# Optimization experiments

Hardware: AMD Instinct MI355X
Metric: run time of the kernel (lower is better)

## Reference

```python
import jax, jax.numpy as jnp
import numpy as np

N_HEADS = 16
D_HEAD = 64
N_ROTATE = 32
ROPE_BASE = 10000.0
MAX_LEN = 2048  # round_up_to_multiple_of_256(keep count); static for jit
BATCH, SEQ = 2, 4096


def setup_inputs() -> dict:
    key = jax.random.key(0)
    kq, kk, kv = jax.random.split(key, 3)
    q = jax.random.normal(kq, (BATCH, N_HEADS, MAX_LEN, D_HEAD), jnp.float32)
    k = jax.random.normal(kk, (BATCH, N_HEADS, SEQ, D_HEAD), jnp.float32)
    v = jax.random.normal(kv, (BATCH, N_HEADS, SEQ, D_HEAD), jnp.float32)
    # causal full mask [batch, seq, seq] and full position ids [batch, seq]
    mask_full = jnp.broadcast_to(jnp.tril(jnp.ones((SEQ, SEQ), bool)), (BATCH, SEQ, SEQ))
    pos_full = jnp.broadcast_to(jnp.arange(SEQ, dtype=jnp.int32), (BATCH, SEQ))
    # skip_mask: exactly MAX_LEN kept tokens per row (random positions)
    rng = np.random.default_rng(0)
    sm = np.zeros((BATCH, SEQ), dtype=bool)
    for i in range(BATCH):
        sm[i, rng.permutation(SEQ)[:MAX_LEN]] = True
    return {"q": q, "k": k, "v": v, "mask_full": mask_full,
            "pos_full": pos_full, "skip_mask": jnp.asarray(sm)}


def _rope_rotate(x, pos):
    # x: [b, h, L, n_rotate], pos: [b, L]
    half = N_ROTATE // 2
    inv_freq = 1.0 / (ROPE_BASE ** (jnp.arange(0, N_ROTATE, 2, dtype=jnp.float32) / N_ROTATE))
    freqs = pos.astype(jnp.float32)[..., None] * inv_freq          # [b, L, half]
    emb = jnp.concatenate([freqs, freqs], axis=-1)[:, None]        # [b, 1, L, n_rotate]
    cos, sin = jnp.cos(emb), jnp.sin(emb)
    x1, x2 = x[..., :half], x[..., half:]
    rot = jnp.concatenate([-x2, x1], axis=-1)                      # rotate_half
    return x * cos + rot * sin


def reference(q, k, v, mask_full, pos_full, skip_mask):
    b, S = skip_mask.shape
    lengths = skip_mask.sum(axis=1)
    # vectorized _trim_attention_mask: stable argsort compacts kept indices to the front
    order = jnp.argsort(jnp.where(skip_mask, 0, 1), axis=1, stable=True)
    idx = order[:, :MAX_LEN]                                       # [b, max_len]
    brow = jnp.arange(b)[:, None]
    mask_trim = mask_full[brow, idx]                               # [b, max_len, S]
    pos_trim = pos_full[brow, idx]                                 # [b, max_len]
    valid = jnp.arange(MAX_LEN)[None, :] < lengths[:, None]
    mask_trim = mask_trim & valid[..., None]
    pos_trim = jnp.where(valid, pos_trim, 0)

    # partial RoPE on first n_rotate channels
    rq = _rope_rotate(q[..., :N_ROTATE], pos_trim)
    rk = _rope_rotate(k[..., :N_ROTATE], pos_full)
    q = jnp.concatenate([rq, q[..., N_ROTATE:]], axis=-1)
    k = jnp.concatenate([rk, k[..., N_ROTATE:]], axis=-1)

    # masked SDPA (bool mask broadcast over heads)
    scale = 1.0 / jnp.sqrt(jnp.float32(D_HEAD))
    scores = jnp.einsum('bhqd,bhkd->bhqk', q, k) * scale
    scores = jnp.where(mask_trim[:, None], scores, jnp.finfo(scores.dtype).min)
    attn = jax.nn.softmax(scores, axis=-1)
    return jnp.einsum('bhqk,bhkd->bhqd', attn, v)
```

## Files before the change

kernel.cpp:

```cpp
#include <hip/hip_runtime.h>
#include <math.h>

#define BB 2
#define HH 16
#define QQ 2048
#define SS 4096
#define DD 64
#define NRH 16
#define NQT 32
#define PBPAD 68

typedef unsigned short u16;
typedef unsigned int   u32;
typedef short bhalf8 __attribute__((ext_vector_type(8)));
typedef float f32x4  __attribute__((ext_vector_type(4)));

typedef __attribute__((address_space(1))) const u32 gu32;
typedef __attribute__((address_space(3))) u32 lu32;

#if __has_builtin(__builtin_amdgcn_exp2f)
#define EXP2(x) __builtin_amdgcn_exp2f(x)
#else
#define EXP2(x) exp2f(x)
#endif

union Frag16 { uint4 u; bhalf8 v; u16 s[8]; uint2 d[2]; };

__device__ __forceinline__ u16 f2bf(float f) {
  union { float f; u32 u; } c; c.f = f;
  return (u16)((c.u + 0x7FFFu + ((c.u >> 16) & 1u)) >> 16);
}

__device__ __forceinline__ bhalf8 ldfrag(const u16* p) {
  Frag16 f; f.u = *reinterpret_cast<const uint4*>(p); return f.v;
}

__device__ __forceinline__ void rope32(float* x, int pos) {
  const float step = 0.8304820237218405f;
  const float fp = (float)pos;
#pragma unroll
  for (int i = 0; i < NRH; ++i) {
    float ang = fp * exp2f(-step * (float)i);
    float sv, cv;
    __sincosf(ang, &sv, &cv);
    float a = x[i], b = x[i + NRH];
    x[i]       = a * cv - b * sv;
    x[i + NRH] = b * cv + a * sv;
  }
}

__global__ void prep_idx_kernel(const unsigned char* __restrict__ sm,
                                int* __restrict__ idx) {
  __shared__ int wsum[4];
  __shared__ int modes;
  const int tid = threadIdx.x;
  const int b = (int)blockIdx.x;

  int c = 0;
  for (int i = 0; i < 32; ++i) c += (sm[tid * 32 + i] != 0) ? 1 : 0;
#pragma unroll
  for (int off = 32; off; off >>= 1) c += __shfl_down(c, off);
  if ((tid & 63) == 0) wsum[tid >> 6] = c;
  __syncthreads();
  if (tid == 0) modes = (wsum[0] + wsum[1] + wsum[2] + wsum[3] > 3000) ? 1 : 0;
  __syncthreads();
  const bool byteMode = (modes != 0);
  const u32* sm32 = (const u32*)sm;

  const int base = b * SS + tid * 16;
  u32 flags = 0;
  for (int i = 0; i < 16; ++i) {
    bool f = byteMode ? (sm[base + i] != 0) : (sm32[base + i] != 0);
    flags |= ((u32)(f ? 1 : 0)) << i;
  }
  int cnt = __popc(flags);
  int vv = cnt;
#pragma unroll
  for (int off = 1; off < 64; off <<= 1) {
    int t = __shfl_up(vv, off);
    if ((tid & 63) >= off) vv += t;
  }
  __syncthreads();
  if ((tid & 63) == 63) wsum[tid >> 6] = vv;
  __syncthreads();
  int add = 0;
  for (int w2 = 0; w2 < (tid >> 6); ++w2) add += wsum[w2];
  int p = vv - cnt + add;
  for (int i = 0; i < 16; ++i) {
    if (flags & (1u << i)) {
      if (p < QQ) idx[b * QQ + p] = tid * 16 + i;
      ++p;
    }
  }
}

__global__ __launch_bounds__(256) void prep_kv_kernel(const float* __restrict__ k,
                                                      const float* __restrict__ v,
                                                      u16* __restrict__ kbf,
                                                      u16* __restrict__ vt) {
  __shared__ u16 tile[64][72];
  if (blockIdx.x < 512) {
    int r = blockIdx.x * 256 + threadIdx.x;
    int pos = r & (SS - 1);
    float x[64];
    const float4* src = (const float4*)(k + (size_t)r * DD);
#pragma unroll
    for (int i = 0; i < 16; ++i) {
      float4 t = src[i];
      x[4 * i] = t.x; x[4 * i + 1] = t.y; x[4 * i + 2] = t.z; x[4 * i + 3] = t.w;
    }
    rope32(x, pos);
    u16 tmp[64];
#pragma unroll
    for (int i = 0; i < 64; ++i) tmp[i] = f2bf(x[i]);
    uint4* dst = (uint4*)(kbf + (size_t)r * DD);
#pragma unroll
    for (int i = 0; i < 8; ++i) dst[i] = ((uint4*)tmp)[i];
  } else {
    int blk = (int)blockIdx.x - 512;
    int bh = blk >> 6;
    int jt = blk & 63;
    int t = threadIdx.x;
    int jl = t >> 2;
    int dc = (t & 3) * 16;
    const float4* src = (const float4*)(v + ((size_t)(bh * SS + jt * 64 + jl)) * DD + dc);
#pragma unroll
    for (int i = 0; i < 4; ++i) {
      float4 f = src[i];
      tile[jl][dc + 4 * i]     = f2bf(f.x);
      tile[jl][dc + 4 * i + 1] = f2bf(f.y);
      tile[jl][dc + 4 * i + 2] = f2bf(f.z);
      tile[jl][dc + 4 * i + 3] = f2bf(f.w);
    }
    __syncthreads();
    int d = t >> 2;
    int js = (t & 3) * 16;
    u16 o[16];
#pragma unroll
    for (int i = 0; i < 16; ++i) o[i] = tile[js + i][d];
    uint4* dst = (uint4*)(vt + ((size_t)(bh * DD + d)) * SS + jt * 64 + js);
    dst[0] = ((uint4*)o)[0];
    dst[1] = ((uint4*)o)[1];
  }
}

__device__ __forceinline__ void stage_tiles(const char* kb_bh, const char* vt_bh,
                                            u16* Kb, u16* Vb, int t0,
                                            int w, int srow, int schk) {
#pragma unroll
  for (int p2 = 0; p2 < 2; ++p2) {
    const int rr = w * 16 + p2 * 8 + srow;
    {
      const char* g = kb_bh + (size_t)(t0 + rr) * 128 + ((schk ^ (rr & 7)) * 16);
      lu32* l = (lu32*)((char*)Kb + (w * 16 + p2 * 8) * 128);
      __builtin_amdgcn_global_load_lds((gu32*)g, l, 16, 0, 0);
    }
    {
      const char* g = vt_bh + (size_t)rr * (SS * 2) + t0 * 2 + ((schk ^ (rr & 7)) * 16);
      lu32* l = (lu32*)((char*)Vb + (w * 16 + p2 * 8) * 128);
      __builtin_amdgcn_global_load_lds((gu32*)g, l, 16, 0, 0);
    }
  }
}

__device__ __forceinline__ void attn_tile(
    const u16* __restrict__ Kb, const u16* __restrict__ Vb, u16* __restrict__ pb,
    int t0, int grp, int col,
    int bnd0, int bnd1, int bnd2, int bnd3,
    bhalf8 qa0, bhalf8 qa1,
    f32x4& acc0, f32x4& acc1, f32x4& acc2, f32x4& acc3,
    float& l0, float& l1, float& l2, float& l3) {
  const int swz = col & 7;
  f32x4 s0 = {0.f, 0.f, 0.f, 0.f}, s1 = s0, s2 = s0, s3 = s0;
  {
    const u16* kr0 = Kb + (0 * 16 + col) * 64;
    const u16* kr1 = Kb + (1 * 16 + col) * 64;
    const u16* kr2 = Kb + (2 * 16 + col) * 64;
    const u16* kr3 = Kb + (3 * 16 + col) * 64;
    s0 = __builtin_amdgcn_mfma_f32_16x16x32_bf16(qa0, ldfrag(kr0 + ((grp ^ swz) * 8)), s0, 0, 0, 0);
    s1 = __builtin_amdgcn_mfma_f32_16x16x32_bf16(qa0, ldfrag(kr1 + ((grp ^ swz) * 8)), s1, 0, 0, 0);
    s2 = __builtin_amdgcn_mfma_f32_16x16x32_bf16(qa0, ldfrag(kr2 + ((grp ^ swz) * 8)), s2, 0, 0, 0);
    s3 = __builtin_amdgcn_mfma_f32_16x16x32_bf16(qa0, ldfrag(kr3 + ((grp ^ swz) * 8)), s3, 0, 0, 0);
    s0 = __builtin_amdgcn_mfma_f32_16x16x32_bf16(qa1, ldfrag(kr0 + (((4 + grp) ^ swz) * 8)), s0, 0, 0, 0);
    s1 = __builtin_amdgcn_mfma_f32_16x16x32_bf16(qa1, ldfrag(kr1 + (((4 + grp) ^ swz) * 8)), s1, 0, 0, 0);
    s2 = __builtin_amdgcn_mfma_f32_16x16x32_bf16(qa1, ldfrag(kr2 + (((4 + grp) ^ swz) * 8)), s2, 0, 0, 0);
    s3 = __builtin_amdgcn_mfma_f32_16x16x32_bf16(qa1, ldfrag(kr3 + (((4 + grp) ^ swz) * 8)), s3, 0, 0, 0);
  }

  const int key0 = t0 + col, key1 = t0 + 16 + col, key2 = t0 + 32 + col, key3 = t0 + 48 + col;
#define SM_ROW(R, BND, LACC)                                                   \
  {                                                                            \
    float p0 = (key0 <= (BND)) ? EXP2(s0[R] - 16.f) : 0.f;                     \
    float p1 = (key1 <= (BND)) ? EXP2(s1[R] - 16.f) : 0.f;                     \
    float p2v = (key2 <= (BND)) ? EXP2(s2[R] - 16.f) : 0.f;                    \
    float p3 = (key3 <= (BND)) ? EXP2(s3[R] - 16.f) : 0.f;                     \
    (LACC) += (p0 + p1) + (p2v + p3);                                          \
    u16* prow = pb + (grp * 4 + (R)) * PBPAD;                                  \
    prow[col] = f2bf(p0); prow[16 + col] = f2bf(p1);                           \
    prow[32 + col] = f2bf(p2v); prow[48 + col] = f2bf(p3);                     \
  }
  SM_ROW(0, bnd0, l0)
  SM_ROW(1, bnd1, l1)
  SM_ROW(2, bnd2, l2)
  SM_ROW(3, bnd3, l3)
#undef SM_ROW

  bhalf8 pa0, pa1;
  {
    const u16* p = pb + col * PBPAD;
    Frag16 f0, f1;
    f0.d[0] = *(const uint2*)(p + grp * 8);
    f0.d[1] = *(const uint2*)(p + grp * 8 + 4);
    f1.d[0] = *(const uint2*)(p + 32 + grp * 8);
    f1.d[1] = *(const uint2*)(p + 32 + grp * 8 + 4);
    pa0 = f0.v; pa1 = f1.v;
  }

  {
    const u16* vr0 = Vb + (0 * 16 + col) * 64;
    const u16* vr1 = Vb + (1 * 16 + col) * 64;
    const u16* vr2 = Vb + (2 * 16 + col) * 64;
    const u16* vr3 = Vb + (3 * 16 + col) * 64;
    acc0 = __builtin_amdgcn_mfma_f32_16x16x32_bf16(pa0, ldfrag(vr0 + ((grp ^ swz) * 8)), acc0, 0, 0, 0);
    acc1 = __builtin_amdgcn_mfma_f32_16x16x32_bf16(pa0, ldfrag(vr1 + ((grp ^ swz) * 8)), acc1, 0, 0, 0);
    acc2 = __builtin_amdgcn_mfma_f32_16x16x32_bf16(pa0, ldfrag(vr2 + ((grp ^ swz) * 8)), acc2, 0, 0, 0);
    acc3 = __builtin_amdgcn_mfma_f32_16x16x32_bf16(pa0, ldfrag(vr3 + ((grp ^ swz) * 8)), acc3, 0, 0, 0);
    acc0 = __builtin_amdgcn_mfma_f32_16x16x32_bf16(pa1, ldfrag(vr0 + (((4 + grp) ^ swz) * 8)), acc0, 0, 0, 0);
    acc1 = __builtin_amdgcn_mfma_f32_16x16x32_bf16(pa1, ldfrag(vr1 + (((4 + grp) ^ swz) * 8)), acc1, 0, 0, 0);
    acc2 = __builtin_amdgcn_mfma_f32_16x16x32_bf16(pa1, ldfrag(vr2 + (((4 + grp) ^ swz) * 8)), acc2, 0, 0, 0);
    acc3 = __builtin_amdgcn_mfma_f32_16x16x32_bf16(pa1, ldfrag(vr3 + (((4 + grp) ^ swz) * 8)), acc3, 0, 0, 0);
  }
}

__global__ __launch_bounds__(256) void attn_mfma_kernel(
    const float* __restrict__ qsrc, const u16* __restrict__ kbf,
    const u16* __restrict__ vt, const int* __restrict__ idx,
    float* __restrict__ out) {
  __shared__ u16 KbufA[64 * 64];
  __shared__ u16 VbufA[64 * 64];
  __shared__ u16 KbufB[64 * 64];
  __shared__ u16 VbufB[64 * 64];
  __shared__ u16 Pbuf[4][16 * PBPAD];

  const int blk = (int)blockIdx.x;
  const int bh  = blk & 31;
  const int pr  = blk >> 5;
  const int b   = bh >> 4;
  const int tid  = threadIdx.x;
  const int w    = tid >> 6;
  const int lane = tid & 63;
  const int grp  = lane >> 4;
  const int col  = lane & 15;

  const char* kb_bh = (const char*)(kbf + (size_t)bh * SS * DD);
  const char* vt_bh = (const char*)(vt + (size_t)bh * DD * SS);

  const int srow = lane >> 3;
  const int schk = lane & 7;

  u16* pb = Pbuf[w];

  for (int pass = 0; pass < 2; ++pass) {
    const int qt = pass ? (NQT - 1 - pr) : pr;
    const int q0 = qt * 64;

    const int bnd0 = idx[b * QQ + q0 + w * 16 + grp * 4 + 0];
    const int bnd1 = idx[b * QQ + q0 + w * 16 + grp * 4 + 1];
    const int bnd2 = idx[b * QQ + q0 + w * 16 + grp * 4 + 2];
    const int bnd3 = idx[b * QQ + q0 + w * 16 + grp * 4 + 3];
    const int maxbound = idx[b * QQ + q0 + 63];
    const int ntiles = (maxbound >> 6) + 1;

    bhalf8 qa0, qa1;
    {
      const int qrow = q0 + w * 16 + col;
      const int mypos = idx[b * QQ + qrow];
      const float* qr = qsrc + (size_t)(bh * QQ + qrow) * DD;
      const int lof = (grp & 1) * 8;
      float4 A0 = *(const float4*)(qr + lof);
      float4 A1 = *(const float4*)(qr + lof + 4);
      float4 B0 = *(const float4*)(qr + 16 + lof);
      float4 B1 = *(const float4*)(qr + 16 + lof + 4);
      float4 C0 = *(const float4*)(qr + 32 + grp * 8);
      float4 C1 = *(const float4*)(qr + 32 + grp * 8 + 4);
      float xlo[8] = {A0.x, A0.y, A0.z, A0.w, A1.x, A1.y, A1.z, A1.w};
      float xhi[8] = {B0.x, B0.y, B0.z, B0.w, B1.x, B1.y, B1.z, B1.w};
      float xq1[8] = {C0.x, C0.y, C0.z, C0.w, C1.x, C1.y, C1.z, C1.w};
      const float scq = 0.125f * 1.44269504088896f;
      const float fp = (float)mypos;
      Frag16 f0, f1;
#pragma unroll
      for (int j = 0; j < 8; ++j) {
        float ang = fp * exp2f(-0.8304820237218405f * (float)(lof + j));
        float sv, cv;
        __sincosf(ang, &sv, &cv);
        float val = (grp >= 2) ? (xhi[j] * cv + xlo[j] * sv)
                               : (xlo[j] * cv - xhi[j] * sv);
        f0.s[j] = f2bf(val * scq);
        f1.s[j] = f2bf(xq1[j] * scq);
      }
      qa0 = f0.v; qa1 = f1.v;
    }

    f32x4 acc0 = {0.f, 0.f, 0.f, 0.f}, acc1 = acc0, acc2 = acc0, acc3 = acc0;
    float l0 = 0.f, l1 = 0.f, l2 = 0.f, l3 = 0.f;

    stage_tiles(kb_bh, vt_bh, KbufA, VbufA, 0, w, srow, schk);
    __syncthreads();

    for (int ti = 0; ti < ntiles; ti += 2) {
      const bool has1 = (ti + 1) < ntiles;
      if (has1) stage_tiles(kb_bh, vt_bh, KbufB, VbufB, (ti + 1) << 6, w, srow, schk);
      attn_tile(KbufA, VbufA, pb, ti << 6, grp, col, bnd0, bnd1, bnd2, bnd3,
                qa0, qa1, acc0, acc1, acc2, acc3, l0, l1, l2, l3);
      __syncthreads();
      if (has1) {
        if (ti + 2 < ntiles)
          stage_tiles(kb_bh, vt_bh, KbufA, VbufA, (ti + 2) << 6, w, srow, schk);
        attn_tile(KbufB, VbufB, pb, (ti + 1) << 6, grp, col, bnd0, bnd1, bnd2, bnd3,
                  qa0, qa1, acc0, acc1, acc2, acc3, l0, l1, l2, l3);
        __syncthreads();
      }
    }

#pragma unroll
    for (int mdel = 1; mdel < 16; mdel <<= 1) {
      l0 += __shfl_xor(l0, mdel);
      l1 += __shfl_xor(l1, mdel);
      l2 += __shfl_xor(l2, mdel);
      l3 += __shfl_xor(l3, mdel);
    }
    float i0 = 1.f / l0, i1 = 1.f / l1, i2 = 1.f / l2, i3 = 1.f / l3;
    float* ob = out + (size_t)(bh * QQ + q0 + w * 16 + grp * 4) * DD + col;
#pragma unroll
    for (int r = 0; r < 4; ++r) {
      float iv = (r == 0) ? i0 : (r == 1) ? i1 : (r == 2) ? i2 : i3;
      ob[(size_t)r * DD + 0]  = acc0[r] * iv;
      ob[(size_t)r * DD + 16] = acc1[r] * iv;
      ob[(size_t)r * DD + 32] = acc2[r] * iv;
      ob[(size_t)r * DD + 48] = acc3[r] * iv;
    }
  }
}

__global__ __launch_bounds__(64) void attn_fb_kernel(const float* __restrict__ q,
                                                     const float* __restrict__ ksrc,
                                                     const float* __restrict__ v,
                                                     const int* __restrict__ idx,
                                                     float* __restrict__ out) {
  int t = (int)(gridDim.x - 1u - blockIdx.x);
  int sub = t >> 5;
  int bh = t & 31;
  int b = bh >> 4;
  int lane = threadIdx.x;
  int qi = sub * 64 + lane;
  const int bound = idx[b * QQ + qi];

  float qreg[64];
  {
    const float4* qp = (const float4*)(q + ((size_t)bh * QQ + qi) * DD);
#pragma unroll
    for (int i = 0; i < 16; ++i) {
      float4 t4 = qp[i];
      qreg[4 * i] = t4.x; qreg[4 * i + 1] = t4.y;
      qreg[4 * i + 2] = t4.z; qreg[4 * i + 3] = t4.w;
    }
  }
  rope32(qreg, bound);
#pragma unroll
  for (int i = 0; i < 64; ++i) qreg[i] *= 0.125f;

  const float* kbase = ksrc + (size_t)bh * SS * DD;
  const float* vbase = v + (size_t)bh * SS * DD;
  float acc[64];
#pragma unroll
  for (int i = 0; i < 64; ++i) acc[i] = 0.f;
  float mrun = -INFINITY, lrun = 0.f;

  for (int j = 0; j <= bound; ++j) {
    float ka[64];
    const float4* kp = (const float4*)(kbase + (size_t)j * DD);
#pragma unroll
    for (int i = 0; i < 16; ++i) {
      float4 t4 = kp[i];
      ka[4 * i] = t4.x; ka[4 * i + 1] = t4.y;
      ka[4 * i + 2] = t4.z; ka[4 * i + 3] = t4.w;
    }
    rope32(ka, j);
    float s0 = 0.f, s1 = 0.f, s2 = 0.f, s3 = 0.f;
#pragma unroll
    for (int i = 0; i < 16; ++i) {
      s0 = fmaf(qreg[4 * i], ka[4 * i], s0);
      s1 = fmaf(qreg[4 * i + 1], ka[4 * i + 1], s1);
      s2 = fmaf(qreg[4 * i + 2], ka[4 * i + 2], s2);
      s3 = fmaf(qreg[4 * i + 3], ka[4 * i + 3], s3);
    }
    float sc = (s0 + s1) + (s2 + s3);
    if (sc > mrun) {
      float alpha = __expf(mrun - sc);
      lrun *= alpha;
#pragma unroll
      for (int i = 0; i < 64; ++i) acc[i] *= alpha;
      mrun = sc;
    }
    float pw = __expf(sc - mrun);
    lrun += pw;
    const float4* vp = (const float4*)(vbase + (size_t)j * DD);
#pragma unroll
    for (int i = 0; i < 16; ++i) {
      float4 t4 = vp[i];
      acc[4 * i] = fmaf(pw, t4.x, acc[4 * i]);
      acc[4 * i + 1] = fmaf(pw, t4.y, acc[4 * i + 1]);
      acc[4 * i + 2] = fmaf(pw, t4.z, acc[4 * i + 2]);
      acc[4 * i + 3] = fmaf(pw, t4.w, acc[4 * i + 3]);
    }
  }
  float inv = 1.0f / lrun;
  float4* op = (float4*)(out + ((size_t)bh * QQ + qi) * DD);
#pragma unroll
  for (int i = 0; i < 16; ++i) {
    float4 t4;
    t4.x = acc[4 * i] * inv; t4.y = acc[4 * i + 1] * inv;
    t4.z = acc[4 * i + 2] * inv; t4.w = acc[4 * i + 3] * inv;
    op[i] = t4;
  }
}

extern "C" void kernel_launch(void* const* d_in, const int* in_sizes, int n_in,
                              void* d_out, int out_size, void* d_ws, size_t ws_size,
                              hipStream_t stream) {
  (void)in_sizes; (void)n_in; (void)out_size;
  const float* q = (const float*)d_in[0];
  const float* k = (const float*)d_in[1];
  const float* v = (const float*)d_in[2];
  const unsigned char* skip = (const unsigned char*)d_in[5];
  float* out = (float*)d_out;

  char* base = (char*)d_ws;
  int* idx = (int*)base;
  const size_t kbytes = (size_t)BB * HH * SS * DD * 2;
  u16* kbf = (u16*)(base + 16384);
  u16* vtb = (u16*)(base + 16384 + kbytes);
  const size_t need = 16384 + 2 * kbytes;

  prep_idx_kernel<<<2, 256, 0, stream>>>(skip, idx);
  if (ws_size >= need) {
    prep_kv_kernel<<<512 + BB * HH * 64, 256, 0, stream>>>(k, v, kbf, vtb);
    attn_mfma_kernel<<<(NQT / 2) * 32, 256, 0, stream>>>(q, kbf, vtb, idx, out);
  } else {
    attn_fb_kernel<<<1024, 64, 0, stream>>>(q, k, v, idx, out);
  }
}
```

Measured before the change: 316.5 us.

## Split query passes into separate blocks, skip fully masked tiles, pack P writes

```diff
diff --git a/kernel.cpp b/kernel.cpp
--- a/kernel.cpp
+++ b/kernel.cpp
@@ -8,7 +8,6 @@
 #define DD 64
 #define NRH 16
 #define NQT 32
-#define PBPAD 68
 
 typedef unsigned short u16;
 typedef unsigned int   u32;
@@ -29,6 +28,12 @@
 __device__ __forceinline__ u16 f2bf(float f) {
   union { float f; u32 u; } c; c.f = f;
   return (u16)((c.u + 0x7FFFu + ((c.u >> 16) & 1u)) >> 16);
+}
+
+__device__ __forceinline__ u32 cvt_pk_bf16(float lo, float hi) {
+  u32 r;
+  asm("v_cvt_pk_bf16_f32 %0, %1, %2" : "=v"(r) : "v"(lo), "v"(hi));
+  return r;
 }
 
 __device__ __forceinline__ bhalf8 ldfrag(const u16* p) {
@@ -134,11 +139,12 @@
     }
     __syncthreads();
     int d = t >> 2;
-    int js = (t & 3) * 16;
+    int c = t & 3;
     u16 o[16];
 #pragma unroll
-    for (int i = 0; i < 16; ++i) o[i] = tile[js + i][d];
-    uint4* dst = (uint4*)(vt + ((size_t)(bh * DD + d)) * SS + jt * 64 + js);
+    for (int m = 0; m < 16; ++m)
+      o[m] = tile[4 * c + (m >> 2) + ((m & 3) << 4)][d];
+    uint4* dst = (uint4*)(vt + ((size_t)(bh * DD + d)) * SS + jt * 64 + c * 16);
     dst[0] = ((uint4*)o)[0];
     dst[1] = ((uint4*)o)[1];
   }
@@ -163,10 +169,13 @@
   }
 }
 
+template <bool MASKED>
 __device__ __forceinline__ void attn_tile(
     const u16* __restrict__ Kb, const u16* __restrict__ Vb, u16* __restrict__ pb,
     int t0, int grp, int col,
     int bnd0, int bnd1, int bnd2, int bnd3,
+    int paIdx0, int paIdx1,
+    int pwIdx0, int pwIdx1, int pwIdx2, int pwIdx3,
     bhalf8 qa0, bhalf8 qa1,
     f32x4& acc0, f32x4& acc1, f32x4& acc2, f32x4& acc3,
     float& l0, float& l1, float& l2, float& l3) {
@@ -177,6 +186,7 @@
     const u16* kr1 = Kb + (1 * 16 + col) * 64;
     const u16* kr2 = Kb + (2 * 16 + col) * 64;
     const u16* kr3 = Kb + (3 * 16 + col) * 64;
+    __builtin_amdgcn_s_setprio(1);
     s0 = __builtin_amdgcn_mfma_f32_16x16x32_bf16(qa0, ldfrag(kr0 + ((grp ^ swz) * 8)), s0, 0, 0, 0);
     s1 = __builtin_amdgcn_mfma_f32_16x16x32_bf16(qa0, ldfrag(kr1 + ((grp ^ swz) * 8)), s1, 0, 0, 0);
     s2 = __builtin_amdgcn_mfma_f32_16x16x32_bf16(qa0, ldfrag(kr2 + ((grp ^ swz) * 8)), s2, 0, 0, 0);
@@ -185,34 +195,41 @@
     s1 = __builtin_amdgcn_mfma_f32_16x16x32_bf16(qa1, ldfrag(kr1 + (((4 + grp) ^ swz) * 8)), s1, 0, 0, 0);
     s2 = __builtin_amdgcn_mfma_f32_16x16x32_bf16(qa1, ldfrag(kr2 + (((4 + grp) ^ swz) * 8)), s2, 0, 0, 0);
     s3 = __builtin_amdgcn_mfma_f32_16x16x32_bf16(qa1, ldfrag(kr3 + (((4 + grp) ^ swz) * 8)), s3, 0, 0, 0);
-  }
-
-  const int key0 = t0 + col, key1 = t0 + 16 + col, key2 = t0 + 32 + col, key3 = t0 + 48 + col;
-#define SM_ROW(R, BND, LACC)                                                   \
+    __builtin_amdgcn_s_setprio(0);
+  }
+
+  const int key0 = t0 + col;
+#define SM_ROW(R, BND, LACC, PWI)                                              \
   {                                                                            \
-    float p0 = (key0 <= (BND)) ? EXP2(s0[R] - 16.f) : 0.f;                     \
-    float p1 = (key1 <= (BND)) ? EXP2(s1[R] - 16.f) : 0.f;                     \
-    float p2v = (key2 <= (BND)) ? EXP2(s2[R] - 16.f) : 0.f;                    \
-    float p3 = (key3 <= (BND)) ? EXP2(s3[R] - 16.f) : 0.f;                     \
+    float p0, p1, p2v, p3;                                                     \
+    if (MASKED) {                                                              \
+      p0  = (key0      <= (BND)) ? EXP2(s0[R] - 16.f) : 0.f;                   \
+      p1  = (key0 + 16 <= (BND)) ? EXP2(s1[R] - 16.f) : 0.f;                   \
+      p2v = (key0 + 32 <= (BND)) ? EXP2(s2[R] - 16.f) : 0.f;                   \
+      p3  = (key0 + 48 <= (BND)) ? EXP2(s3[R] - 16.f) : 0.f;                   \
+    } else {                                                                   \
+      p0  = EXP2(s0[R] - 16.f);                                                \
+      p1  = EXP2(s1[R] - 16.f);                                                \
+      p2v = EXP2(s2[R] - 16.f);                                                \
+      p3  = EXP2(s3[R] - 16.f);                                                \
+    }                                                                          \
     (LACC) += (p0 + p1) + (p2v + p3);                                          \
-    u16* prow = pb + (grp * 4 + (R)) * PBPAD;                                  \
-    prow[col] = f2bf(p0); prow[16 + col] = f2bf(p1);                           \
-    prow[32 + col] = f2bf(p2v); prow[48 + col] = f2bf(p3);                     \
-  }
-  SM_ROW(0, bnd0, l0)
-  SM_ROW(1, bnd1, l1)
-  SM_ROW(2, bnd2, l2)
-  SM_ROW(3, bnd3, l3)
+    uint2 pw;                                                                  \
+    pw.x = cvt_pk_bf16(p0, p1);                                                \
+    pw.y = cvt_pk_bf16(p2v, p3);                                               \
+    *(uint2*)(pb + (PWI)) = pw;                                                \
+  }
+  SM_ROW(0, bnd0, l0, pwIdx0)
+  SM_ROW(1, bnd1, l1, pwIdx1)
+  SM_ROW(2, bnd2, l2, pwIdx2)
+  SM_ROW(3, bnd3, l3, pwIdx3)
 #undef SM_ROW
 
   bhalf8 pa0, pa1;
   {
-    const u16* p = pb + col * PBPAD;
     Frag16 f0, f1;
-    f0.d[0] = *(const uint2*)(p + grp * 8);
-    f0.d[1] = *(const uint2*)(p + grp * 8 + 4);
-    f1.d[0] = *(const uint2*)(p + 32 + grp * 8);
-    f1.d[1] = *(const uint2*)(p + 32 + grp * 8 + 4);
+    f0.u = *(const uint4*)(pb + paIdx0);
+    f1.u = *(const uint4*)(pb + paIdx1);
     pa0 = f0.v; pa1 = f1.v;
   }
 
@@ -221,6 +238,7 @@
     const u16* vr1 = Vb + (1 * 16 + col) * 64;
     const u16* vr2 = Vb + (2 * 16 + col) * 64;
     const u16* vr3 = Vb + (3 * 16 + col) * 64;
+    __builtin_amdgcn_s_setprio(1);
     acc0 = __builtin_amdgcn_mfma_f32_16x16x32_bf16(pa0, ldfrag(vr0 + ((grp ^ swz) * 8)), acc0, 0, 0, 0);
     acc1 = __builtin_amdgcn_mfma_f32_16x16x32_bf16(pa0, ldfrag(vr1 + ((grp ^ swz) * 8)), acc1, 0, 0, 0);
     acc2 = __builtin_amdgcn_mfma_f32_16x16x32_bf16(pa0, ldfrag(vr2 + ((grp ^ swz) * 8)), acc2, 0, 0, 0);
@@ -229,10 +247,11 @@
     acc1 = __builtin_amdgcn_mfma_f32_16x16x32_bf16(pa1, ldfrag(vr1 + (((4 + grp) ^ swz) * 8)), acc1, 0, 0, 0);
     acc2 = __builtin_amdgcn_mfma_f32_16x16x32_bf16(pa1, ldfrag(vr2 + (((4 + grp) ^ swz) * 8)), acc2, 0, 0, 0);
     acc3 = __builtin_amdgcn_mfma_f32_16x16x32_bf16(pa1, ldfrag(vr3 + (((4 + grp) ^ swz) * 8)), acc3, 0, 0, 0);
-  }
-}
-
-__global__ __launch_bounds__(256) void attn_mfma_kernel(
+    __builtin_amdgcn_s_setprio(0);
+  }
+}
+
+__global__ __launch_bounds__(256, 4) void attn_mfma_kernel(
     const float* __restrict__ qsrc, const u16* __restrict__ kbf,
     const u16* __restrict__ vt, const int* __restrict__ idx,
     float* __restrict__ out) {
@@ -240,11 +259,12 @@
   __shared__ u16 VbufA[64 * 64];
   __shared__ u16 KbufB[64 * 64];
   __shared__ u16 VbufB[64 * 64];
-  __shared__ u16 Pbuf[4][16 * PBPAD];
+  __shared__ __align__(16) u16 Pbuf[4][16 * 64];
 
   const int blk = (int)blockIdx.x;
   const int bh  = blk & 31;
-  const int pr  = blk >> 5;
+  const int qt  = (NQT - 1) - (blk >> 5);
+  const int q0  = qt * 64;
   const int b   = bh >> 4;
   const int tid  = threadIdx.x;
   const int w    = tid >> 6;
@@ -260,86 +280,114 @@
 
   u16* pb = Pbuf[w];
 
-  for (int pass = 0; pass < 2; ++pass) {
-    const int qt = pass ? (NQT - 1 - pr) : pr;
-    const int q0 = qt * 64;
-
-    const int bnd0 = idx[b * QQ + q0 + w * 16 + grp * 4 + 0];
-    const int bnd1 = idx[b * QQ + q0 + w * 16 + grp * 4 + 1];
-    const int bnd2 = idx[b * QQ + q0 + w * 16 + grp * 4 + 2];
-    const int bnd3 = idx[b * QQ + q0 + w * 16 + grp * 4 + 3];
-    const int maxbound = idx[b * QQ + q0 + 63];
-    const int ntiles = (maxbound >> 6) + 1;
-
-    bhalf8 qa0, qa1;
+  const int* idxb = idx + b * QQ + q0;
+  const int bnd0 = idxb[w * 16 + grp * 4 + 0];
+  const int bnd1 = idxb[w * 16 + grp * 4 + 1];
+  const int bnd2 = idxb[w * 16 + grp * 4 + 2];
+  const int bnd3 = idxb[w * 16 + grp * 4 + 3];
+  const int wave_minb = idxb[w * 16];
+  const int wave_maxb = idxb[w * 16 + 15];
+  const int maxbound  = idxb[63];
+  const int ntiles = (maxbound >> 6) + 1;
+
+  const int paIdx0 = col * 64 + ((grp ^ (col & 7)) << 3);
+  const int paIdx1 = col * 64 + (((grp + 4) ^ (col & 7)) << 3);
+  const int qg = grp * 4;
+  const int pwIdx0 = (qg + 0) * 64 + ((((col >> 1) ^ ((qg + 0) & 7))) << 3) + ((col & 1) << 2);
+  const int pwIdx1 = (qg + 1) * 64 + ((((col >> 1) ^ ((qg + 1) & 7))) << 3) + ((col & 1) << 2);
+  const int pwIdx2 = (qg + 2) * 64 + ((((col >> 1) ^ ((qg + 2) & 7))) << 3) + ((col & 1) << 2);
+  const int pwIdx3 = (qg + 3) * 64 + ((((col >> 1) ^ ((qg + 3) & 7))) << 3) + ((col & 1) << 2);
+
+  bhalf8 qa0, qa1;
+  {
+    const int qrow = q0 + w * 16 + col;
+    const int mypos = idx[b * QQ + qrow];
+    const float* qr = qsrc + (size_t)(bh * QQ + qrow) * DD;
+    const int lof = (grp & 1) * 8;
+    float4 A0 = *(const float4*)(qr + lof);
+    float4 A1 = *(const float4*)(qr + lof + 4);
+    float4 B0 = *(const float4*)(qr + 16 + lof);
+    float4 B1 = *(const float4*)(qr + 16 + lof + 4);
+    float4 C0 = *(const float4*)(qr + 32 + grp * 8);
+    float4 C1 = *(const float4*)(qr + 32 + grp * 8 + 4);
+    float xlo[8] = {A0.x, A0.y, A0.z, A0.w, A1.x, A1.y, A1.z, A1.w};
+    float xhi[8] = {B0.x, B0.y, B0.z, B0.w, B1.x, B1.y, B1.z, B1.w};
+    float xq1[8] = {C0.x, C0.y, C0.z, C0.w, C1.x, C1.y, C1.z, C1.w};
+    const float scq = 0.125f * 1.44269504088896f;
+    const float fp = (float)mypos;
+    Frag16 f0, f1;
+#pragma unroll
+    for (int j = 0; j < 8; ++j) {
+      float ang = fp * exp2f(-0.8304820237218405f * (float)(lof + j));
+      float sv, cv;
+      __sincosf(ang, &sv, &cv);
+      float val = (grp >= 2) ? (xhi[j] * cv + xlo[j] * sv)
+                             : (xlo[j] * cv - xhi[j] * sv);
+      f0.s[j] = f2bf(val * scq);
+      f1.s[j] = f2bf(xq1[j] * scq);
+    }
+    qa0 = f0.v; qa1 = f1.v;
+  }
+
+  f32x4 acc0 = {0.f, 0.f, 0.f, 0.f}, acc1 = acc0, acc2 = acc0, acc3 = acc0;
+  float l0 = 0.f, l1 = 0.f, l2 = 0.f, l3 = 0.f;
+
+  stage_tiles(kb_bh, vt_bh, KbufA, VbufA, 0, w, srow, schk);
+  __syncthreads();
+
+  for (int ti = 0; ti < ntiles; ti += 2) {
+    const bool has1 = (ti + 1) < ntiles;
+    if (has1) stage_tiles(kb_bh, vt_bh, KbufB, VbufB, (ti + 1) << 6, w, srow, schk);
     {
-      const int qrow = q0 + w * 16 + col;
-      const int mypos = idx[b * QQ + qrow];
-      const float* qr = qsrc + (size_t)(bh * QQ + qrow) * DD;
-      const int lof = (grp & 1) * 8;
-      float4 A0 = *(const float4*)(qr + lof);
-      float4 A1 = *(const float4*)(qr + lof + 4);
-      float4 B0 = *(const float4*)(qr + 16 + lof);
-      float4 B1 = *(const float4*)(qr + 16 + lof + 4);
-      float4 C0 = *(const float4*)(qr + 32 + grp * 8);
-      float4 C1 = *(const float4*)(qr + 32 + grp * 8 + 4);
-      float xlo[8] = {A0.x, A0.y, A0.z, A0.w, A1.x, A1.y, A1.z, A1.w};
-      float xhi[8] = {B0.x, B0.y, B0.z, B0.w, B1.x, B1.y, B1.z, B1.w};
-      float xq1[8] = {C0.x, C0.y, C0.z, C0.w, C1.x, C1.y, C1.z, C1.w};
-      const float scq = 0.125f * 1.44269504088896f;
-      const float fp = (float)mypos;
-      Frag16 f0, f1;
-#pragma unroll
-      for (int j = 0; j < 8; ++j) {
-        float ang = fp * exp2f(-0.8304820237218405f * (float)(lof + j));
-        float sv, cv;
-        __sincosf(ang, &sv, &cv);
-        float val = (grp >= 2) ? (xhi[j] * cv + xlo[j] * sv)
-                               : (xlo[j] * cv - xhi[j] * sv);
-        f0.s[j] = f2bf(val * scq);
-        f1.s[j] = f2bf(xq1[j] * scq);
+      const int t0 = ti << 6;
+      if (t0 <= wave_maxb) {
+        if (t0 + 63 <= wave_minb)
+          attn_tile<false>(KbufA, VbufA, pb, t0, grp, col, bnd0, bnd1, bnd2, bnd3,
+                           paIdx0, paIdx1, pwIdx0, pwIdx1, pwIdx2, pwIdx3,
+                           qa0, qa1, acc0, acc1, acc2, acc3, l0, l1, l2, l3);
+        else
+          attn_tile<true>(KbufA, VbufA, pb, t0, grp, col, bnd0, bnd1, bnd2, bnd3,
+                          paIdx0, paIdx1, pwIdx0, pwIdx1, pwIdx2, pwIdx3,
+                          qa0, qa1, acc0, acc1, acc2, acc3, l0, l1, l2, l3);
       }
-      qa0 = f0.v; qa1 = f1.v;
-    }
-
-    f32x4 acc0 = {0.f, 0.f, 0.f, 0.f}, acc1 = acc0, acc2 = acc0, acc3 = acc0;
-    float l0 = 0.f, l1 = 0.f, l2 = 0.f, l3 = 0.f;
-
-    stage_tiles(kb_bh, vt_bh, KbufA, VbufA, 0, w, srow, schk);
+    }
     __syncthreads();
-
-    for (int ti = 0; ti < ntiles; ti += 2) {
-      const bool has1 = (ti + 1) < ntiles;
-      if (has1) stage_tiles(kb_bh, vt_bh, KbufB, VbufB, (ti + 1) << 6, w, srow, schk);
-      attn_tile(KbufA, VbufA, pb, ti << 6, grp, col, bnd0, bnd1, bnd2, bnd3,
-                qa0, qa1, acc0, acc1, acc2, acc3, l0, l1, l2, l3);
+    if (has1) {
+      if (ti + 2 < ntiles)
+        stage_tiles(kb_bh, vt_bh, KbufA, VbufA, (ti + 2) << 6, w, srow, schk);
+      {
+        const int t0 = (ti + 1) << 6;
+        if (t0 <= wave_maxb) {
+          if (t0 + 63 <= wave_minb)
+            attn_tile<false>(KbufB, VbufB, pb, t0, grp, col, bnd0, bnd1, bnd2, bnd3,
+                             paIdx0, paIdx1, pwIdx0, pwIdx1, pwIdx2, pwIdx3,
+                             qa0, qa1, acc0, acc1, acc2, acc3, l0, l1, l2, l3);
+          else
+            attn_tile<true>(KbufB, VbufB, pb, t0, grp, col, bnd0, bnd1, bnd2, bnd3,
+                            paIdx0, paIdx1, pwIdx0, pwIdx1, pwIdx2, pwIdx3,
+                            qa0, qa1, acc0, acc1, acc2, acc3, l0, l1, l2, l3);
+        }
+      }
       __syncthreads();
-      if (has1) {
-        if (ti + 2 < ntiles)
-          stage_tiles(kb_bh, vt_bh, KbufA, VbufA, (ti + 2) << 6, w, srow, schk);
-        attn_tile(KbufB, VbufB, pb, (ti + 1) << 6, grp, col, bnd0, bnd1, bnd2, bnd3,
-                  qa0, qa1, acc0, acc1, acc2, acc3, l0, l1, l2, l3);
-        __syncthreads();
-      }
-    }
-
-#pragma unroll
-    for (int mdel = 1; mdel < 16; mdel <<= 1) {
-      l0 += __shfl_xor(l0, mdel);
-      l1 += __shfl_xor(l1, mdel);
-      l2 += __shfl_xor(l2, mdel);
-      l3 += __shfl_xor(l3, mdel);
-    }
-    float i0 = 1.f / l0, i1 = 1.f / l1, i2 = 1.f / l2, i3 = 1.f / l3;
-    float* ob = out + (size_t)(bh * QQ + q0 + w * 16 + grp * 4) * DD + col;
-#pragma unroll
-    for (int r = 0; r < 4; ++r) {
-      float iv = (r == 0) ? i0 : (r == 1) ? i1 : (r == 2) ? i2 : i3;
-      ob[(size_t)r * DD + 0]  = acc0[r] * iv;
-      ob[(size_t)r * DD + 16] = acc1[r] * iv;
-      ob[(size_t)r * DD + 32] = acc2[r] * iv;
-      ob[(size_t)r * DD + 48] = acc3[r] * iv;
-    }
+    }
+  }
+
+#pragma unroll
+  for (int mdel = 1; mdel < 16; mdel <<= 1) {
+    l0 += __shfl_xor(l0, mdel);
+    l1 += __shfl_xor(l1, mdel);
+    l2 += __shfl_xor(l2, mdel);
+    l3 += __shfl_xor(l3, mdel);
+  }
+  float i0 = 1.f / l0, i1 = 1.f / l1, i2 = 1.f / l2, i3 = 1.f / l3;
+  float* ob = out + (size_t)(bh * QQ + q0 + w * 16 + grp * 4) * DD + col;
+#pragma unroll
+  for (int r = 0; r < 4; ++r) {
+    float iv = (r == 0) ? i0 : (r == 1) ? i1 : (r == 2) ? i2 : i3;
+    ob[(size_t)r * DD + 0]  = acc0[r] * iv;
+    ob[(size_t)r * DD + 16] = acc1[r] * iv;
+    ob[(size_t)r * DD + 32] = acc2[r] * iv;
+    ob[(size_t)r * DD + 48] = acc3[r] * iv;
   }
 }
 
@@ -446,7 +494,7 @@
   prep_idx_kernel<<<2, 256, 0, stream>>>(skip, idx);
   if (ws_size >= need) {
     prep_kv_kernel<<<512 + BB * HH * 64, 256, 0, stream>>>(k, v, kbf, vtb);
-    attn_mfma_kernel<<<(NQT / 2) * 32, 256, 0, stream>>>(q, kbf, vtb, idx, out);
+    attn_mfma_kernel<<<NQT * 32, 256, 0, stream>>>(q, kbf, vtb, idx, out);
   } else {
     attn_fb_kernel<<<1024, 64, 0, stream>>>(q, k, v, idx, out);
   }
```

Measured after the change: 296.8 us. -6.2%, faster.
